# Kernel tuning notes

Hardware: AMD Instinct MI355X
Metric: run time of the kernel (lower is better)

Reference implementation:

```python
import jax, jax.numpy as jnp
import numpy as np

B, N, K, D = 8, 4096, 26, 64


def setup_inputs() -> dict:
    key = jax.random.key(0)
    ks = jax.random.split(key, 7)
    return {
        "targets": jax.random.normal(ks[0], (B, N, D), dtype=jnp.float32),
        "neighbors": jax.random.normal(ks[1], (B, N, K, D), dtype=jnp.float32),
        "a": jax.random.uniform(ks[2], (B, N, K), dtype=jnp.float32),
        "kernel_target": jax.random.normal(ks[3], (1, 1, D), dtype=jnp.float32) * 0.1,
        "bias_target": jax.random.normal(ks[4], (1, 1, D), dtype=jnp.float32) * 0.1,
        "kernel_neighbor": jax.random.normal(ks[5], (1, 1, D), dtype=jnp.float32) * 0.1,
        "bias_neighbor": jax.random.normal(ks[6], (1, 1, 1, D), dtype=jnp.float32) * 0.1,
    }


def reference(targets, neighbors, a, kernel_target, bias_target, kernel_neighbor, bias_neighbor):
    # Faithful to the TF call(), including the broadcast quirk:
    # targets (B,N,D) * kernel_neighbor (1,1,D) + bias_neighbor (1,1,1,D) -> (1,B,N,D)
    t = targets * kernel_neighbor + bias_neighbor            # (1,B,N,D)
    n = neighbors * kernel_target + bias_target              # (B,N,K,D)
    # expand_dims(t, -2) -> (1,B,N,1,D); product with n and a[...,None] -> (1,B,N,K,D);
    # reduce_sum over axis=2 (the N axis of the rank-5 tensor) -> (1,B,K,D).
    # Expressed as a fused einsum to avoid materializing the rank-5 intermediate.
    w = jnp.einsum("zbnd,bnkd,bnk->zbkd", t, n, a)           # (1,B,K,D)
    return jax.nn.sigmoid(w)
```

## Files before the change

kernel.cpp:

```cpp
#include <hip/hip_runtime.h>
#include <math.h>

#define BB 8
#define NN 4096
#define KK 26
#define DD 64
#define CH 128
#define NPB (NN / CH)
#define KD (KK * DD)
#define KD4 (KD / 4)

__global__ __launch_bounds__(256) void gat_partial_ws(
    const float* __restrict__ targets,
    const float* __restrict__ neighbors,
    const float* __restrict__ a,
    const float* __restrict__ kt, const float* __restrict__ bt,
    const float* __restrict__ kn, const float* __restrict__ bn,
    float* __restrict__ ws)
{
    const int b     = blockIdx.x / CH;
    const int chunk = blockIdx.x % CH;
    const int tid   = threadIdx.x;
    const int wave  = tid >> 6;
    const int lane  = tid & 63;

    const int g16 = lane >> 4, r16 = lane & 15;
    const int g32 = lane >> 5, r32 = lane & 31;

    const float4 kt4 = ((const float4*)kt)[r16];
    const float4 bt4 = ((const float4*)bt)[r16];
    const float4 kn4 = ((const float4*)kn)[r16];
    const float4 bn4 = ((const float4*)bn)[r16];
    const float2 kt2 = ((const float2*)kt)[r32];
    const float2 bt2 = ((const float2*)bt)[r32];
    const float2 kn2 = ((const float2*)kn)[r32];
    const float2 bn2 = ((const float2*)bn)[r32];

    float4 acc4[6];
#pragma unroll
    for (int kk = 0; kk < 6; ++kk) acc4[kk] = make_float4(0.f, 0.f, 0.f, 0.f);
    float2 accT = make_float2(0.f, 0.f);

    const int n0 = chunk * NPB;
    for (int n = n0 + wave; n < n0 + NPB; n += 4) {
        const size_t row = (size_t)(b * NN + n);
        const float4 t4 = ((const float4*)(targets + row * DD))[r16];
        const float2 t2 = ((const float2*)(targets + row * DD))[r32];
        float4 tt4;
        tt4.x = fmaf(t4.x, kn4.x, bn4.x);
        tt4.y = fmaf(t4.y, kn4.y, bn4.y);
        tt4.z = fmaf(t4.z, kn4.z, bn4.z);
        tt4.w = fmaf(t4.w, kn4.w, bn4.w);
        float2 tt2;
        tt2.x = fmaf(t2.x, kn2.x, bn2.x);
        tt2.y = fmaf(t2.y, kn2.y, bn2.y);

        const float4* __restrict__ nbrow4 = (const float4*)(neighbors + row * (size_t)KD);
        const float*  __restrict__ arow   = a + row * KK;
#pragma unroll
        for (int kk = 0; kk < 6; ++kk) {
            const float  av = arow[kk * 4 + g16];
            const float4 v  = nbrow4[kk * 64 + lane];
            acc4[kk].x = fmaf(tt4.x * av, fmaf(v.x, kt4.x, bt4.x), acc4[kk].x);
            acc4[kk].y = fmaf(tt4.y * av, fmaf(v.y, kt4.y, bt4.y), acc4[kk].y);
            acc4[kk].z = fmaf(tt4.z * av, fmaf(v.z, kt4.z, bt4.z), acc4[kk].z);
            acc4[kk].w = fmaf(tt4.w * av, fmaf(v.w, kt4.w, bt4.w), acc4[kk].w);
        }
        {
            const float  av = arow[24 + g32];
            const float2 v  = ((const float2*)nbrow4)[768 + lane];
            accT.x = fmaf(tt2.x * av, fmaf(v.x, kt2.x, bt2.x), accT.x);
            accT.y = fmaf(tt2.y * av, fmaf(v.y, kt2.y, bt2.y), accT.y);
        }
    }

    __shared__ float lds[4][KD];
#pragma unroll
    for (int kk = 0; kk < 6; ++kk)
        ((float4*)lds[wave])[kk * 64 + lane] = acc4[kk];
    ((float2*)lds[wave])[768 + lane] = accT;
    __syncthreads();

    float4* __restrict__ wrow4 = (float4*)(ws + ((size_t)b * CH + chunk) * KD);
    for (int i4 = tid; i4 < KD4; i4 += 256) {
        const float4 v0 = ((const float4*)lds[0])[i4];
        const float4 v1 = ((const float4*)lds[1])[i4];
        const float4 v2 = ((const float4*)lds[2])[i4];
        const float4 v3 = ((const float4*)lds[3])[i4];
        float4 s;
        s.x = (v0.x + v1.x) + (v2.x + v3.x);
        s.y = (v0.y + v1.y) + (v2.y + v3.y);
        s.z = (v0.z + v1.z) + (v2.z + v3.z);
        s.w = (v0.w + v1.w) + (v2.w + v3.w);
        wrow4[i4] = s;
    }
}

__global__ __launch_bounds__(256) void gat_reduce_sigmoid(
    const float* __restrict__ ws, float* __restrict__ out)
{
    const int b    = blockIdx.x / 13;
    const int jblk = blockIdx.x % 13;
    const int tid  = threadIdx.x;
    const int o    = tid & 31;
    const int g    = tid >> 5;

    const float4* __restrict__ ws4 = (const float4*)ws;
    const size_t base = (size_t)b * CH * KD4 + (size_t)jblk * 32 + o;

    float4 s = make_float4(0.f, 0.f, 0.f, 0.f);
#pragma unroll
    for (int i = 0; i < CH / 8; ++i) {
        const int c = g + i * 8;
        const float4 v = ws4[base + (size_t)c * KD4];
        s.x += v.x; s.y += v.y; s.z += v.z; s.w += v.w;
    }

    __shared__ float4 lds4[8][32];
    lds4[g][o] = s;
    __syncthreads();

    if (tid < 32) {
        float4 t = lds4[0][o];
#pragma unroll
        for (int gg = 1; gg < 8; ++gg) {
            const float4 v = lds4[gg][o];
            t.x += v.x; t.y += v.y; t.z += v.z; t.w += v.w;
        }
        float4 oo;
        oo.x = 1.f / (1.f + expf(-t.x));
        oo.y = 1.f / (1.f + expf(-t.y));
        oo.z = 1.f / (1.f + expf(-t.z));
        oo.w = 1.f / (1.f + expf(-t.w));
        ((float4*)out)[(size_t)b * KD4 + (size_t)jblk * 32 + o] = oo;
    }
}

__global__ __launch_bounds__(256) void gat_partial_atomic(
    const float* __restrict__ targets, const float* __restrict__ neighbors,
    const float* __restrict__ a,
    const float* __restrict__ kt, const float* __restrict__ bt,
    const float* __restrict__ kn, const float* __restrict__ bn,
    float* __restrict__ out)
{
    const int b     = blockIdx.x / CH;
    const int chunk = blockIdx.x % CH;
    const int tid   = threadIdx.x;
    const int wave  = tid >> 6;
    const int lane  = tid & 63;
    const int d     = lane;
    const float kt_d = kt[d], bt_d = bt[d], kn_d = kn[d], bn_d = bn[d];
    float acc[KK];
#pragma unroll
    for (int k = 0; k < KK; ++k) acc[k] = 0.f;
    const int n0 = chunk * NPB;
    for (int n = n0 + wave; n < n0 + NPB; n += 4) {
        const size_t row = (size_t)(b * NN + n);
        const float tt = fmaf(targets[row * DD + d], kn_d, bn_d);
        const float* __restrict__ nbrow = neighbors + row * (size_t)KD;
        const float* __restrict__ arow  = a + row * KK;
#pragma unroll
        for (int k = 0; k < KK; ++k)
            acc[k] = fmaf(tt * arow[k], fmaf(nbrow[k * DD + d], kt_d, bt_d), acc[k]);
    }
    __shared__ float lds[4][KD];
#pragma unroll
    for (int k = 0; k < KK; ++k) lds[wave][k * DD + lane] = acc[k];
    __syncthreads();
    for (int idx = tid; idx < KD; idx += 256) {
        const float s = lds[0][idx] + lds[1][idx] + lds[2][idx] + lds[3][idx];
        atomicAdd(&out[b * KD + idx], s);
    }
}

__global__ __launch_bounds__(256) void gat_sigmoid(float* __restrict__ out, int nelem) {
    const int i = blockIdx.x * blockDim.x + threadIdx.x;
    if (i < nelem) out[i] = 1.f / (1.f + expf(-out[i]));
}

extern "C" void kernel_launch(void* const* d_in, const int* in_sizes, int n_in,
                              void* d_out, int out_size, void* d_ws, size_t ws_size,
                              hipStream_t stream) {
    const float* targets   = (const float*)d_in[0];
    const float* neighbors = (const float*)d_in[1];
    const float* a         = (const float*)d_in[2];
    const float* kt        = (const float*)d_in[3];
    const float* bt        = (const float*)d_in[4];
    const float* kn        = (const float*)d_in[5];
    const float* bn        = (const float*)d_in[6];
    float* out = (float*)d_out;

    const size_t ws_need = (size_t)BB * CH * KD * sizeof(float);
    if (ws_size >= ws_need) {
        float* ws = (float*)d_ws;
        gat_partial_ws<<<BB * CH, 256, 0, stream>>>(targets, neighbors, a, kt, bt, kn, bn, ws);
        gat_reduce_sigmoid<<<BB * 13, 256, 0, stream>>>(ws, out);
    } else {
        hipMemsetAsync(d_out, 0, (size_t)out_size * sizeof(float), stream);
        gat_partial_atomic<<<BB * CH, 256, 0, stream>>>(targets, neighbors, a, kt, bt, kn, bn, out);
        gat_sigmoid<<<(out_size + 255) / 256, 256, 0, stream>>>(out, out_size);
    }
}
```

Baseline: 42.03 us.

## Fuse partial and reduce kernels using last-block arrival counter and spin-wait

Merges the partial-sum and final reduce+sigmoid kernels into one launch. Each block increments a per-batch counter after writing its partial; the last 13 arriving blocks spin until all partials are written, then each reduces one slice and applies sigmoid. This removes a kernel launch boundary but adds a memset, atomics and a spin-wait that assumes co-residency of blocks.

```diff
diff --git a/kernel.cpp b/kernel.cpp
--- a/kernel.cpp
+++ b/kernel.cpp
@@ -9,14 +9,21 @@
 #define NPB (NN / CH)
 #define KD (KK * DD)
 #define KD4 (KD / 4)
-
-__global__ __launch_bounds__(256) void gat_partial_ws(
+#define NSLICE 13
+
+#define WS_PART_FLOATS (BB * CH * KD)
+#define WS_CNT_OFF     ((size_t)WS_PART_FLOATS * 4)
+#define WS_BYTES       (WS_CNT_OFF + BB * 4)
+
+__global__ __launch_bounds__(256) void gat_fused2(
     const float* __restrict__ targets,
     const float* __restrict__ neighbors,
     const float* __restrict__ a,
     const float* __restrict__ kt, const float* __restrict__ bt,
     const float* __restrict__ kn, const float* __restrict__ bn,
-    float* __restrict__ ws)
+    float* __restrict__ ws,
+    int*   __restrict__ cnt,
+    float* __restrict__ out)
 {
     const int b     = blockIdx.x / CH;
     const int chunk = blockIdx.x % CH;
@@ -94,6 +101,138 @@
         s.w = (v0.w + v1.w) + (v2.w + v3.w);
         wrow4[i4] = s;
     }
+
+    __threadfence();
+    __shared__ int sh_ret;
+    if (tid == 0) sh_ret = atomicAdd(&cnt[b], 1);
+    __syncthreads();
+    const int ret = sh_ret;
+    if (ret < CH - NSLICE) return;
+
+    const int slice = ret - (CH - NSLICE);
+    if (tid == 0) {
+        while (__hip_atomic_load(&cnt[b], __ATOMIC_RELAXED, __HIP_MEMORY_SCOPE_AGENT) < CH)
+            __builtin_amdgcn_s_sleep(8);
+    }
+    __syncthreads();
+    __threadfence();
+
+    const int o = tid & 31;
+    const int g = tid >> 5;
+    const float4* __restrict__ ws4 = (const float4*)ws;
+    const size_t base = (size_t)b * CH * KD4 + (size_t)slice * 32 + o;
+
+    float4 s = make_float4(0.f, 0.f, 0.f, 0.f);
+#pragma unroll
+    for (int i = 0; i < CH / 8; ++i) {
+        const int c = g + i * 8;
+        const float4 v = ws4[base + (size_t)c * KD4];
+        s.x += v.x; s.y += v.y; s.z += v.z; s.w += v.w;
+    }
+
+    float4* lds4 = (float4*)lds[0];
+    __syncthreads();
+    lds4[g * 32 + o] = s;
+    __syncthreads();
+
+    if (tid < 32) {
+        float4 t = lds4[o];
+#pragma unroll
+        for (int gg = 1; gg < 8; ++gg) {
+            const float4 v = lds4[gg * 32 + o];
+            t.x += v.x; t.y += v.y; t.z += v.z; t.w += v.w;
+        }
+        float4 oo;
+        oo.x = 1.f / (1.f + expf(-t.x));
+        oo.y = 1.f / (1.f + expf(-t.y));
+        oo.z = 1.f / (1.f + expf(-t.z));
+        oo.w = 1.f / (1.f + expf(-t.w));
+        ((float4*)out)[(size_t)b * KD4 + (size_t)slice * 32 + o] = oo;
+    }
+}
+
+__global__ __launch_bounds__(256) void gat_partial_ws(
+    const float* __restrict__ targets, const float* __restrict__ neighbors,
+    const float* __restrict__ a,
+    const float* __restrict__ kt, const float* __restrict__ bt,
+    const float* __restrict__ kn, const float* __restrict__ bn,
+    float* __restrict__ ws)
+{
+    const int b     = blockIdx.x / CH;
+    const int chunk = blockIdx.x % CH;
+    const int tid   = threadIdx.x;
+    const int wave  = tid >> 6;
+    const int lane  = tid & 63;
+    const int g16 = lane >> 4, r16 = lane & 15;
+    const int g32 = lane >> 5, r32 = lane & 31;
+
+    const float4 kt4 = ((const float4*)kt)[r16];
+    const float4 bt4 = ((const float4*)bt)[r16];
+    const float4 kn4 = ((const float4*)kn)[r16];
+    const float4 bn4 = ((const float4*)bn)[r16];
+    const float2 kt2 = ((const float2*)kt)[r32];
+    const float2 bt2 = ((const float2*)bt)[r32];
+    const float2 kn2 = ((const float2*)kn)[r32];
+    const float2 bn2 = ((const float2*)bn)[r32];
+
+    float4 acc4[6];
+#pragma unroll
+    for (int kk = 0; kk < 6; ++kk) acc4[kk] = make_float4(0.f, 0.f, 0.f, 0.f);
+    float2 accT = make_float2(0.f, 0.f);
+
+    const int n0 = chunk * NPB;
+    for (int n = n0 + wave; n < n0 + NPB; n += 4) {
+        const size_t row = (size_t)(b * NN + n);
+        const float4 t4 = ((const float4*)(targets + row * DD))[r16];
+        const float2 t2 = ((const float2*)(targets + row * DD))[r32];
+        float4 tt4;
+        tt4.x = fmaf(t4.x, kn4.x, bn4.x);
+        tt4.y = fmaf(t4.y, kn4.y, bn4.y);
+        tt4.z = fmaf(t4.z, kn4.z, bn4.z);
+        tt4.w = fmaf(t4.w, kn4.w, bn4.w);
+        float2 tt2;
+        tt2.x = fmaf(t2.x, kn2.x, bn2.x);
+        tt2.y = fmaf(t2.y, kn2.y, bn2.y);
+
+        const float4* __restrict__ nbrow4 = (const float4*)(neighbors + row * (size_t)KD);
+        const float*  __restrict__ arow   = a + row * KK;
+#pragma unroll
+        for (int kk = 0; kk < 6; ++kk) {
+            const float  av = arow[kk * 4 + g16];
+            const float4 v  = nbrow4[kk * 64 + lane];
+            acc4[kk].x = fmaf(tt4.x * av, fmaf(v.x, kt4.x, bt4.x), acc4[kk].x);
+            acc4[kk].y = fmaf(tt4.y * av, fmaf(v.y, kt4.y, bt4.y), acc4[kk].y);
+            acc4[kk].z = fmaf(tt4.z * av, fmaf(v.z, kt4.z, bt4.z), acc4[kk].z);
+            acc4[kk].w = fmaf(tt4.w * av, fmaf(v.w, kt4.w, bt4.w), acc4[kk].w);
+        }
+        {
+            const float  av = arow[24 + g32];
+            const float2 v  = ((const float2*)nbrow4)[768 + lane];
+            accT.x = fmaf(tt2.x * av, fmaf(v.x, kt2.x, bt2.x), accT.x);
+            accT.y = fmaf(tt2.y * av, fmaf(v.y, kt2.y, bt2.y), accT.y);
+        }
+    }
+
+    __shared__ float lds[4][KD];
+#pragma unroll
+    for (int kk = 0; kk < 6; ++kk)
+        ((float4*)lds[wave])[kk * 64 + lane] = acc4[kk];
+    ((float2*)lds[wave])[768 + lane] = accT;
+    __syncthreads();
+
+    float4* __restrict__ wrow4 = (float4*)(ws + ((size_t)b * CH + chunk) * KD);
+    for (int i4 = tid; i4 < KD4; i4 += 256) {
+        const float4 v0 = ((const float4*)lds[0])[i4];
+        const float4 v1 = ((const float4*)lds[1])[i4];
+        const float4 v2 = ((const float4*)lds[2])[i4];
+        const float4 v3 = ((const float4*)lds[3])[i4];
+        float4 s;
+        s.x = (v0.x + v1.x) + (v2.x + v3.x);
+        s.y = (v0.y + v1.y) + (v2.y + v3.y);
+        s.z = (v0.z + v1.z) + (v2.z + v3.z);
+        s.w = (v0.w + v1.w) + (v2.w + v3.w);
+        wrow4[i4] = s;
+    }
 }
 
 __global__ __launch_bounds__(256) void gat_reduce_sigmoid(
@@ -134,48 +273,6 @@
         oo.w = 1.f / (1.f + expf(-t.w));
         ((float4*)out)[(size_t)b * KD4 + (size_t)jblk * 32 + o] = oo;
     }
-}
-
-__global__ __launch_bounds__(256) void gat_partial_atomic(
-    const float* __restrict__ targets, const float* __restrict__ neighbors,
-    const float* __restrict__ a,
-    const float* __restrict__ kt, const float* __restrict__ bt,
-    const float* __restrict__ kn, const float* __restrict__ bn,
-    float* __restrict__ out)
-{
-    const int b     = blockIdx.x / CH;
-    const int chunk = blockIdx.x % CH;
-    const int tid   = threadIdx.x;
-    const int wave  = tid >> 6;
-    const int lane  = tid & 63;
-    const int d     = lane;
-    const float kt_d = kt[d], bt_d = bt[d], kn_d = kn[d], bn_d = bn[d];
-    float acc[KK];
-#pragma unroll
-    for (int k = 0; k < KK; ++k) acc[k] = 0.f;
-    const int n0 = chunk * NPB;
-    for (int n = n0 + wave; n < n0 + NPB; n += 4) {
-        const size_t row = (size_t)(b * NN + n);
-        const float tt = fmaf(targets[row * DD + d], kn_d, bn_d);
-        const float* __restrict__ nbrow = neighbors + row * (size_t)KD;
-        const float* __restrict__ arow  = a + row * KK;
-#pragma unroll
-        for (int k = 0; k < KK; ++k)
-            acc[k] = fmaf(tt * arow[k], fmaf(nbrow[k * DD + d], kt_d, bt_d), acc[k]);
-    }
-    __shared__ float lds[4][KD];
-#pragma unroll
-    for (int k = 0; k < KK; ++k) lds[wave][k * DD + lane] = acc[k];
-    __syncthreads();
-    for (int idx = tid; idx < KD; idx += 256) {
-        const float s = lds[0][idx] + lds[1][idx] + lds[2][idx] + lds[3][idx];
-        atomicAdd(&out[b * KD + idx], s);
-    }
-}
-
-__global__ __launch_bounds__(256) void gat_sigmoid(float* __restrict__ out, int nelem) {
-    const int i = blockIdx.x * blockDim.x + threadIdx.x;
-    if (i < nelem) out[i] = 1.f / (1.f + expf(-out[i]));
 }
 
 extern "C" void kernel_launch(void* const* d_in, const int* in_sizes, int n_in,
@@ -190,14 +287,15 @@
     const float* bn        = (const float*)d_in[6];
     float* out = (float*)d_out;
 
-    const size_t ws_need = (size_t)BB * CH * KD * sizeof(float);
-    if (ws_size >= ws_need) {
+    if (ws_size >= WS_BYTES) {
+        float* ws  = (float*)d_ws;
+        int*   cnt = (int*)((char*)d_ws + WS_CNT_OFF);
+        hipMemsetAsync(cnt, 0, BB * sizeof(int), stream);
+        gat_fused2<<<BB * CH, 256, 0, stream>>>(targets, neighbors, a, kt, bt, kn, bn,
+                                                ws, cnt, out);
+    } else {
         float* ws = (float*)d_ws;
         gat_partial_ws<<<BB * CH, 256, 0, stream>>>(targets, neighbors, a, kt, bt, kn, bn, ws);
         gat_reduce_sigmoid<<<BB * 13, 256, 0, stream>>>(ws, out);
-    } else {
-        hipMemsetAsync(d_out, 0, (size_t)out_size * sizeof(float), stream);
-        gat_partial_atomic<<<BB * CH, 256, 0, stream>>>(targets, neighbors, a, kt, bt, kn, bn, out);
-        gat_sigmoid<<<(out_size + 255) / 256, 256, 0, stream>>>(out, out_size);
     }
 }
```

New measurement: 167.0 us. 297% more time.
